# Performance work log

Measured on AMD Instinct MI355X. Metric: run time of the kernel, lower is better.

Reference implementation:

```python
import jax, jax.numpy as jnp
import numpy as np

MARGIN = 0.3

def setup_inputs() -> dict:
    key = jax.random.key(0)
    k1, k2 = jax.random.split(key)
    inputs = jax.random.normal(k1, (4096, 2048), dtype=jnp.float32)
    targets = jax.random.randint(k2, (4096,), 0, 64, dtype=jnp.int64)
    return {"inputs": inputs, "targets": targets}

def reference(inputs, targets):
    # pairwise euclidean distances: [n, n]
    sq = jnp.sum(inputs * inputs, axis=1)
    dist = sq[:, None] + sq[None, :] - 2.0 * (inputs @ inputs.T)
    dist = jnp.sqrt(jnp.clip(dist, 1e-12, None))

    mask = targets[:, None] == targets[None, :]  # same-identity mask, incl. diagonal
    neg_inf = jnp.asarray(-jnp.inf, dist.dtype)

    # soft hard-positive: softmax over positive dists, weighted sum per row
    w_ap = jax.nn.softmax(jnp.where(mask, dist, neg_inf), axis=1)
    dist_ap = jnp.sum(w_ap * dist, axis=1)  # w_ap is 0 on negatives

    # soft hard-negative: softmax over -dist restricted to negatives
    w_an = jax.nn.softmax(jnp.where(mask, neg_inf, -dist), axis=1)
    dist_an = jnp.sum(w_an * dist, axis=1)  # w_an is 0 on positives

    # MarginRankingLoss(dist_an, dist_ap, y=1): mean(max(0, dist_ap - dist_an + margin))
    return jnp.mean(jnp.maximum(dist_ap - dist_an + MARGIN, 0.0))
```

## Files before the change

### kernel.cpp

```cpp
#include <hip/hip_runtime.h>
#include <hip/hip_bf16.h>
#include <stdint.h>

#define N 4096
#define K 2048
#define BM 128
#define BN 128
#define KTB 128
#define NKT (K / KTB)
#define NCB (N / BN)
#define NRB (N / BM)
#define QS 25.4f
#define SCL2 (1.0f / (QS * QS))
#define SHIFT 64.0f

typedef int i32x4 __attribute__((ext_vector_type(4)));
typedef unsigned int u32;

__device__ __forceinline__ void gload16(const void* g, void* l) {
    __builtin_amdgcn_global_load_lds((const __attribute__((address_space(1))) u32*)g,
                                     (__attribute__((address_space(3))) u32*)l, 16, 0, 0);
}

__device__ __forceinline__ int q8(float x) {
    return __float2int_rn(fminf(fmaxf(x * QS, -127.f), 127.f));
}

__global__ __launch_bounds__(256) void k_prep(const float* __restrict__ X,
                                              char* __restrict__ Xq,
                                              float* __restrict__ sq) {
    const int row  = blockIdx.x * 4 + (threadIdx.x >> 6);
    const int lane = threadIdx.x & 63;
    const float4* xr = (const float4*)(X + (size_t)row * K);
    int* qr = (int*)(Xq + (size_t)row * K);
    float s = 0.f;
#pragma unroll
    for (int i = 0; i < 8; ++i) {
        int idx = lane + i * 64;
        float4 v = xr[idx];
        int q0 = q8(v.x), q1 = q8(v.y), q2 = q8(v.z), q3 = q8(v.w);
        s += v.x * v.x + v.y * v.y + v.z * v.z + v.w * v.w;
        qr[idx] = (q0 & 255) | ((q1 & 255) << 8) | ((q2 & 255) << 16) | ((q3 & 255) << 24);
    }
#pragma unroll
    for (int off = 32; off > 0; off >>= 1) s += __shfl_xor(s, off);
    if (lane == 0) sq[row] = s;
}

__global__ __launch_bounds__(256, 4) void k_tile(const char* __restrict__ Xq,
                                                 const int* __restrict__ tg,
                                                 const float* __restrict__ sq,
                                                 float* __restrict__ part) {
    __shared__ __align__(1024) char lds[32768];
    const int tid = threadIdx.x;
    const int cb = blockIdx.x, rb = blockIdx.y;
    const int lane = tid & 63;
    const int wid = tid >> 6;
    const int wr = wid >> 1, wc = wid & 1;
    const int l15 = lane & 15, l4 = lane >> 4;

    const int rsel = lane >> 3;
    const int csel = (lane & 7) ^ rsel;
    const char* gA = Xq + (size_t)(rb * BM + wid * 32 + rsel) * K + csel * 16;
    const char* gB = Xq + (size_t)(cb * BN + wid * 32 + rsel) * K + csel * 16;
    char* ldsA = lds + wid * 4096;
    char* ldsB = lds + 16384 + wid * 4096;

    i32x4 acc[4][4] = {};

    for (int kt = 0; kt < NKT; ++kt) {
        __syncthreads();
        const size_t ko = (size_t)kt * KTB;
#pragma unroll
        for (int j = 0; j < 4; ++j) {
            gload16(gA + ko + (size_t)j * (8 * K), ldsA + j * 1024);
            gload16(gB + ko + (size_t)j * (8 * K), ldsB + j * 1024);
        }
        __syncthreads();
#pragma unroll
        for (int ks = 0; ks < 2; ++ks) {
            i32x4 a[4], b[4];
#pragma unroll
            for (int i = 0; i < 4; ++i) {
                int ar = wr * 64 + i * 16 + l15;
                int ao = ar * 128 + ((((ks << 2) | l4) ^ (ar & 7)) << 4);
                a[i] = *(const i32x4*)(lds + ao);
                int br = wc * 64 + i * 16 + l15;
                int bo = br * 128 + ((((ks << 2) | l4) ^ (br & 7)) << 4);
                b[i] = *(const i32x4*)(lds + 16384 + bo);
            }
#pragma unroll
            for (int at = 0; at < 4; ++at)
#pragma unroll
                for (int ct = 0; ct < 4; ++ct)
                    acc[at][ct] = __builtin_amdgcn_mfma_i32_16x16x64_i8(b[ct], a[at], acc[at][ct], 0, 0, 0);
        }
    }

    float sqc[16]; int tgc[16];
#pragma unroll
    for (int ct = 0; ct < 4; ++ct)
#pragma unroll
        for (int rg = 0; rg < 4; ++rg) {
            int c = cb * BN + wc * 64 + ct * 16 + l4 * 4 + rg;
            sqc[ct * 4 + rg] = sq[c];
            tgc[ct * 4 + rg] = tg[c];
        }
#pragma unroll
    for (int at = 0; at < 4; ++at) {
        int r = rb * BM + wr * 64 + at * 16 + l15;
        float sqr = sq[r];
        int tgr = tg[r];
        float sp = 0.f, tp = 0.f, sn = 0.f, tn = 0.f;
#pragma unroll
        for (int ct = 0; ct < 4; ++ct)
#pragma unroll
            for (int rg = 0; rg < 4; ++rg) {
                float g = SCL2 * (float)acc[at][ct][rg];
                float dd = sqrtf(fmaxf(sqr + sqc[ct * 4 + rg] - 2.0f * g, 1e-12f));
                bool pos = (tgr == tgc[ct * 4 + rg]);
                float e = __expf(pos ? (dd - SHIFT) : (SHIFT - dd));
                float ed = e * dd;
                if (pos) { sp += e; tp += ed; }
                else     { sn += e; tn += ed; }
            }
#pragma unroll
        for (int off = 16; off < 64; off <<= 1) {
            sp += __shfl_xor(sp, off);
            tp += __shfl_xor(tp, off);
            sn += __shfl_xor(sn, off);
            tn += __shfl_xor(tn, off);
        }
        if (l4 == 0) {
            float4 v = {sp, tp, sn, tn};
            *(float4*)(part + (((size_t)(cb * 2 + wc) * N) + r) * 4) = v;
        }
    }
}

__global__ __launch_bounds__(256) void k_final(const float* __restrict__ part,
                                               float* __restrict__ out) {
    int r = blockIdx.x * 256 + threadIdx.x;
    float sp = 0.f, tp = 0.f, sn = 0.f, tn = 0.f;
    for (int s = 0; s < 2 * NCB; ++s) {
        float4 v = *(const float4*)(part + (((size_t)s * N) + r) * 4);
        sp += v.x; tp += v.y; sn += v.z; tn += v.w;
    }
    float h = fmaxf(tp / sp - tn / sn + 0.3f, 0.f);
    __shared__ float red[256];
    red[threadIdx.x] = h;
    __syncthreads();
    for (int k2 = 128; k2 > 0; k2 >>= 1) {
        if (threadIdx.x < k2) red[threadIdx.x] += red[threadIdx.x + k2];
        __syncthreads();
    }
    if (threadIdx.x == 0) atomicAdd(out, red[0] * (1.0f / N));
}

extern "C" void kernel_launch(void* const* d_in, const int* in_sizes, int n_in,
                              void* d_out, int out_size, void* d_ws, size_t ws_size,
                              hipStream_t stream) {
    (void)in_sizes; (void)n_in; (void)out_size; (void)ws_size;
    const float* X  = (const float*)d_in[0];
    const int*   tg = (const int*)d_in[1];

    char* ws = (char*)d_ws;
    float* sq   = (float*)ws;
    float* part = (float*)(ws + 32768);
    char*  Xq   = ws + 4227072;

    hipMemsetAsync(d_out, 0, sizeof(float), stream);
    k_prep<<<N / 4, 256, 0, stream>>>(X, Xq, sq);
    k_tile<<<dim3(NCB, NRB), 256, 0, stream>>>(Xq, tg, sq, part);
    k_final<<<N / 256, 256, 0, stream>>>(part, (float*)d_out);
}
```

Measured before the change: 64.70 us.

## Enlarge GEMM tile to 256x256 with double-buffered LDS and interleaved prefetch

The int8 Gram-matrix kernel moves from 128x128 tiles with 4 waves to 256x256 tiles with 8 waves. LDS is double-buffered at 128KB, and global-to-LDS loads for the next K tile are interleaved between MFMA phases, using explicit barriers, waitcnts and setprio. The aim is more reuse per loaded byte and overlap of memory with matrix math. The cost is a grid of only 256 blocks, higher register pressure from 32 accumulators, and lower occupancy because of the large LDS footprint.

```diff
diff --git a/kernel.cpp b/kernel.cpp
--- a/kernel.cpp
+++ b/kernel.cpp
@@ -4,12 +4,10 @@
 
 #define N 4096
 #define K 2048
-#define BM 128
-#define BN 128
+#define BT 256
 #define KTB 128
 #define NKT (K / KTB)
-#define NCB (N / BN)
-#define NRB (N / BM)
+#define NB (N / BT)
 #define QS 25.4f
 #define SCL2 (1.0f / (QS * QS))
 #define SHIFT 64.0f
@@ -47,78 +45,103 @@
     if (lane == 0) sq[row] = s;
 }
 
-__global__ __launch_bounds__(256, 4) void k_tile(const char* __restrict__ Xq,
+__global__ __launch_bounds__(512, 2) void k_tile(const char* __restrict__ Xq,
                                                  const int* __restrict__ tg,
                                                  const float* __restrict__ sq,
                                                  float* __restrict__ part) {
-    __shared__ __align__(1024) char lds[32768];
+    __shared__ __align__(1024) char lds[131072];
     const int tid = threadIdx.x;
     const int cb = blockIdx.x, rb = blockIdx.y;
     const int lane = tid & 63;
     const int wid = tid >> 6;
-    const int wr = wid >> 1, wc = wid & 1;
+    const int wm = wid >> 2, wn = wid & 3;
     const int l15 = lane & 15, l4 = lane >> 4;
 
     const int rsel = lane >> 3;
     const int csel = (lane & 7) ^ rsel;
-    const char* gA = Xq + (size_t)(rb * BM + wid * 32 + rsel) * K + csel * 16;
-    const char* gB = Xq + (size_t)(cb * BN + wid * 32 + rsel) * K + csel * 16;
-    char* ldsA = lds + wid * 4096;
-    char* ldsB = lds + 16384 + wid * 4096;
+    const char* gA0 = Xq + (size_t)(rb * BT + wid * 8 + rsel) * K + csel * 16;
+    const char* gB0 = Xq + (size_t)(cb * BT + wid * 8 + rsel) * K + csel * 16;
 
-    i32x4 acc[4][4] = {};
+#define GLOAD(j, tile, buf) \
+    gload16(((j) < 4 ? gA0 : gB0) + ((j) & 3) * (64 * K) + (size_t)(tile) * KTB, \
+            (buf) + ((j) < 4 ? 0 : 32768) + ((j) & 3) * 8192 + wid * 1024)
+
+#define RD_A(mh, ks) do { \
+    _Pragma("unroll") for (int i = 0; i < 4; ++i) { \
+        int row = wm * 128 + (mh) * 64 + i * 16 + l15; \
+        a[i] = *(const i32x4*)(bufc + row * 128 + ((((ks) * 4 + l4) ^ (row & 7)) << 4)); } \
+} while (0)
+
+#define RD_B(ks, bb) do { \
+    _Pragma("unroll") for (int i = 0; i < 4; ++i) { \
+        int row = wn * 64 + i * 16 + l15; \
+        bb[i] = *(const i32x4*)(bufc + 32768 + row * 128 + ((((ks) * 4 + l4) ^ (row & 7)) << 4)); } \
+} while (0)
+
+#define MMA(mtb, bb) do { \
+    __builtin_amdgcn_s_setprio(1); \
+    _Pragma("unroll") for (int i = 0; i < 4; ++i) \
+    _Pragma("unroll") for (int nt = 0; nt < 4; ++nt) \
+        acc[(mtb) + i][nt] = __builtin_amdgcn_mfma_i32_16x16x64_i8(bb[nt], a[i], acc[(mtb) + i][nt], 0, 0, 0); \
+    __builtin_amdgcn_s_setprio(0); \
+} while (0)
+
+#define BAR()   __builtin_amdgcn_s_barrier()
+#define LGKM0() do { asm volatile("s_waitcnt lgkmcnt(0)" ::: "memory"); \
+                     __builtin_amdgcn_sched_barrier(0); } while (0)
+#define VM0()   do { asm volatile("s_waitcnt vmcnt(0)" ::: "memory"); \
+                     __builtin_amdgcn_sched_barrier(0); } while (0)
+
+    i32x4 acc[8][4] = {};
+
+    GLOAD(0, 0, lds); GLOAD(1, 0, lds); GLOAD(2, 0, lds); GLOAD(3, 0, lds);
+    GLOAD(4, 0, lds); GLOAD(5, 0, lds); GLOAD(6, 0, lds); GLOAD(7, 0, lds);
+    VM0();
+    BAR();
 
     for (int kt = 0; kt < NKT; ++kt) {
-        __syncthreads();
-        const size_t ko = (size_t)kt * KTB;
-#pragma unroll
-        for (int j = 0; j < 4; ++j) {
-            gload16(gA + ko + (size_t)j * (8 * K), ldsA + j * 1024);
-            gload16(gB + ko + (size_t)j * (8 * K), ldsB + j * 1024);
-        }
-        __syncthreads();
-#pragma unroll
-        for (int ks = 0; ks < 2; ++ks) {
-            i32x4 a[4], b[4];
-#pragma unroll
-            for (int i = 0; i < 4; ++i) {
-                int ar = wr * 64 + i * 16 + l15;
-                int ao = ar * 128 + ((((ks << 2) | l4) ^ (ar & 7)) << 4);
-                a[i] = *(const i32x4*)(lds + ao);
-                int br = wc * 64 + i * 16 + l15;
-                int bo = br * 128 + ((((ks << 2) | l4) ^ (br & 7)) << 4);
-                b[i] = *(const i32x4*)(lds + 16384 + bo);
-            }
-#pragma unroll
-            for (int at = 0; at < 4; ++at)
-#pragma unroll
-                for (int ct = 0; ct < 4; ++ct)
-                    acc[at][ct] = __builtin_amdgcn_mfma_i32_16x16x64_i8(b[ct], a[at], acc[at][ct], 0, 0, 0);
-        }
+        const char* bufc = lds + (kt & 1) * 65536;
+        char* bufn = lds + ((kt + 1) & 1) * 65536;
+        const bool st = (kt + 1 < NKT);
+        i32x4 a[4], b0[4], b1[4];
+        RD_B(0, b0); RD_A(0, 0);
+        if (st) { GLOAD(0, kt + 1, bufn); GLOAD(1, kt + 1, bufn); }
+        BAR(); LGKM0(); MMA(0, b0); BAR();
+        RD_A(1, 0);
+        if (st) { GLOAD(2, kt + 1, bufn); GLOAD(3, kt + 1, bufn); }
+        BAR(); LGKM0(); MMA(4, b0); BAR();
+        RD_B(1, b1); RD_A(0, 1);
+        if (st) { GLOAD(4, kt + 1, bufn); GLOAD(5, kt + 1, bufn); }
+        BAR(); LGKM0(); MMA(0, b1); BAR();
+        RD_A(1, 1);
+        if (st) { GLOAD(6, kt + 1, bufn); GLOAD(7, kt + 1, bufn); }
+        BAR(); LGKM0(); MMA(4, b1);
+        VM0();
+        BAR();
     }
 
     float sqc[16]; int tgc[16];
 #pragma unroll
-    for (int ct = 0; ct < 4; ++ct)
+    for (int nt = 0; nt < 4; ++nt)
 #pragma unroll
         for (int rg = 0; rg < 4; ++rg) {
-            int c = cb * BN + wc * 64 + ct * 16 + l4 * 4 + rg;
-            sqc[ct * 4 + rg] = sq[c];
-            tgc[ct * 4 + rg] = tg[c];
+            int c = cb * BT + wn * 64 + nt * 16 + l4 * 4 + rg;
+            sqc[nt * 4 + rg] = sq[c];
+            tgc[nt * 4 + rg] = tg[c];
         }
 #pragma unroll
-    for (int at = 0; at < 4; ++at) {
-        int r = rb * BM + wr * 64 + at * 16 + l15;
+    for (int mt = 0; mt < 8; ++mt) {
+        int r = rb * BT + wm * 128 + mt * 16 + l15;
         float sqr = sq[r];
         int tgr = tg[r];
         float sp = 0.f, tp = 0.f, sn = 0.f, tn = 0.f;
 #pragma unroll
-        for (int ct = 0; ct < 4; ++ct)
+        for (int nt = 0; nt < 4; ++nt)
 #pragma unroll
             for (int rg = 0; rg < 4; ++rg) {
-                float g = SCL2 * (float)acc[at][ct][rg];
-                float dd = sqrtf(fmaxf(sqr + sqc[ct * 4 + rg] - 2.0f * g, 1e-12f));
-                bool pos = (tgr == tgc[ct * 4 + rg]);
+                float g = SCL2 * (float)acc[mt][nt][rg];
+                float dd = sqrtf(fmaxf(sqr + sqc[nt * 4 + rg] - 2.0f * g, 1e-12f));
+                bool pos = (tgr == tgc[nt * 4 + rg]);
                 float e = __expf(pos ? (dd - SHIFT) : (SHIFT - dd));
                 float ed = e * dd;
                 if (pos) { sp += e; tp += ed; }
@@ -133,7 +156,7 @@
         }
         if (l4 == 0) {
             float4 v = {sp, tp, sn, tn};
-            *(float4*)(part + (((size_t)(cb * 2 + wc) * N) + r) * 4) = v;
+            *(float4*)(part + (((size_t)(cb * 4 + wn) * N) + r) * 4) = v;
         }
     }
 }
@@ -142,7 +165,7 @@
                                                float* __restrict__ out) {
     int r = blockIdx.x * 256 + threadIdx.x;
     float sp = 0.f, tp = 0.f, sn = 0.f, tn = 0.f;
-    for (int s = 0; s < 2 * NCB; ++s) {
+    for (int s = 0; s < 64; ++s) {
         float4 v = *(const float4*)(part + (((size_t)s * N) + r) * 4);
         sp += v.x; tp += v.y; sn += v.z; tn += v.w;
     }
@@ -171,6 +194,6 @@
 
     hipMemsetAsync(d_out, 0, sizeof(float), stream);
     k_prep<<<N / 4, 256, 0, stream>>>(X, Xq, sq);
-    k_tile<<<dim3(NCB, NRB), 256, 0, stream>>>(Xq, tg, sq, part);
+    k_tile<<<dim3(NB, NB), 512, 0, stream>>>(Xq, tg, sq, part);
     k_final<<<N / 256, 256, 0, stream>>>(part, (float*)d_out);
 }
```

Measured after the change: 64.71 us. About the same (+0.0%).

## Exploit Gram matrix symmetry by computing only upper-triangular tiles

Applied to the files above, without the earlier changes.

Launches only upper-triangle tile pairs (rb<=cb) and maps the linear block index to a (rb,cb) pair with a small loop. Each off-diagonal tile computes its epilogue twice, once reduced along rows for row rb and once along columns for the transposed contribution to row cb. This roughly halves the int8 MFMA GEMM work in exchange for a heavier epilogue (double exp/sqrt) on off-diagonal tiles and a serial index-decode loop. Partial slots are laid out so each row still receives exactly 2*NRB contributions.

```diff
diff --git a/kernel.cpp b/kernel.cpp
--- a/kernel.cpp
+++ b/kernel.cpp
@@ -5,11 +5,11 @@
 #define N 4096
 #define K 2048
 #define BM 128
-#define BN 128
 #define KTB 128
 #define NKT (K / KTB)
-#define NCB (N / BN)
 #define NRB (N / BM)
+#define NTILES (NRB * (NRB + 1) / 2)
+#define SLOTS (2 * NRB)
 #define QS 25.4f
 #define SCL2 (1.0f / (QS * QS))
 #define SHIFT 64.0f
@@ -53,7 +53,10 @@
                                                  float* __restrict__ part) {
     __shared__ __align__(1024) char lds[32768];
     const int tid = threadIdx.x;
-    const int cb = blockIdx.x, rb = blockIdx.y;
+    int tt = blockIdx.x, rb = 0;
+    while (tt >= NRB - rb) { tt -= NRB - rb; ++rb; }
+    const int cb = rb + tt;
+
     const int lane = tid & 63;
     const int wid = tid >> 6;
     const int wr = wid >> 1, wc = wid & 1;
@@ -62,7 +65,7 @@
     const int rsel = lane >> 3;
     const int csel = (lane & 7) ^ rsel;
     const char* gA = Xq + (size_t)(rb * BM + wid * 32 + rsel) * K + csel * 16;
-    const char* gB = Xq + (size_t)(cb * BN + wid * 32 + rsel) * K + csel * 16;
+    const char* gB = Xq + (size_t)(cb * BM + wid * 32 + rsel) * K + csel * 16;
     char* ldsA = lds + wid * 4096;
     char* ldsB = lds + 16384 + wid * 4096;
 
@@ -102,23 +105,28 @@
     for (int ct = 0; ct < 4; ++ct)
 #pragma unroll
         for (int rg = 0; rg < 4; ++rg) {
-            int c = cb * BN + wc * 64 + ct * 16 + l4 * 4 + rg;
+            int c = cb * BM + wc * 64 + ct * 16 + l4 * 4 + rg;
             sqc[ct * 4 + rg] = sq[c];
             tgc[ct * 4 + rg] = tg[c];
         }
+    float sqr[4]; int tgr[4];
 #pragma unroll
     for (int at = 0; at < 4; ++at) {
         int r = rb * BM + wr * 64 + at * 16 + l15;
-        float sqr = sq[r];
-        int tgr = tg[r];
+        sqr[at] = sq[r];
+        tgr[at] = tg[r];
+    }
+
+#pragma unroll
+    for (int at = 0; at < 4; ++at) {
         float sp = 0.f, tp = 0.f, sn = 0.f, tn = 0.f;
 #pragma unroll
         for (int ct = 0; ct < 4; ++ct)
 #pragma unroll
             for (int rg = 0; rg < 4; ++rg) {
                 float g = SCL2 * (float)acc[at][ct][rg];
-                float dd = sqrtf(fmaxf(sqr + sqc[ct * 4 + rg] - 2.0f * g, 1e-12f));
-                bool pos = (tgr == tgc[ct * 4 + rg]);
+                float dd = sqrtf(fmaxf(sqr[at] + sqc[ct * 4 + rg] - 2.0f * g, 1e-12f));
+                bool pos = (tgr[at] == tgc[ct * 4 + rg]);
                 float e = __expf(pos ? (dd - SHIFT) : (SHIFT - dd));
                 float ed = e * dd;
                 if (pos) { sp += e; tp += ed; }
@@ -132,9 +140,43 @@
             tn += __shfl_xor(tn, off);
         }
         if (l4 == 0) {
+            int r = rb * BM + wr * 64 + at * 16 + l15;
             float4 v = {sp, tp, sn, tn};
             *(float4*)(part + (((size_t)(cb * 2 + wc) * N) + r) * 4) = v;
         }
+    }
+
+    if (cb != rb) {
+#pragma unroll
+        for (int ct = 0; ct < 4; ++ct)
+#pragma unroll
+            for (int rg = 0; rg < 4; ++rg) {
+                float cS = sqc[ct * 4 + rg];
+                int   cT = tgc[ct * 4 + rg];
+                float sp = 0.f, tp = 0.f, sn = 0.f, tn = 0.f;
+#pragma unroll
+                for (int at = 0; at < 4; ++at) {
+                    float g = SCL2 * (float)acc[at][ct][rg];
+                    float dd = sqrtf(fmaxf(sqr[at] + cS - 2.0f * g, 1e-12f));
+                    bool pos = (tgr[at] == cT);
+                    float e = __expf(pos ? (dd - SHIFT) : (SHIFT - dd));
+                    float ed = e * dd;
+                    if (pos) { sp += e; tp += ed; }
+                    else     { sn += e; tn += ed; }
+                }
+#pragma unroll
+                for (int off = 1; off < 16; off <<= 1) {
+                    sp += __shfl_xor(sp, off);
+                    tp += __shfl_xor(tp, off);
+                    sn += __shfl_xor(sn, off);
+                    tn += __shfl_xor(tn, off);
+                }
+                if (l15 == 0) {
+                    int c = cb * BM + wc * 64 + ct * 16 + l4 * 4 + rg;
+                    float4 v = {sp, tp, sn, tn};
+                    *(float4*)(part + (((size_t)(rb * 2 + wr) * N) + c) * 4) = v;
+                }
+            }
     }
 }
 
@@ -142,7 +184,7 @@
                                                float* __restrict__ out) {
     int r = blockIdx.x * 256 + threadIdx.x;
     float sp = 0.f, tp = 0.f, sn = 0.f, tn = 0.f;
-    for (int s = 0; s < 2 * NCB; ++s) {
+    for (int s = 0; s < SLOTS; ++s) {
         float4 v = *(const float4*)(part + (((size_t)s * N) + r) * 4);
         sp += v.x; tp += v.y; sn += v.z; tn += v.w;
     }
@@ -171,6 +213,6 @@
 
     hipMemsetAsync(d_out, 0, sizeof(float), stream);
     k_prep<<<N / 4, 256, 0, stream>>>(X, Xq, sq);
-    k_tile<<<dim3(NCB, NRB), 256, 0, stream>>>(Xq, tg, sq, part);
+    k_tile<<<NTILES, 256, 0, stream>>>(Xq, tg, sq, part);
     k_final<<<N / 256, 256, 0, stream>>>(part, (float*)d_out);
 }
```

Result: slower. 66.30 us (+2.5%).

## Switch to 32x32x32 int8 MFMA and remap blocks for XCD-aware L2 locality

Applied to the files above, without the earlier changes.

Replaces the 16x16x64 int8 MFMA tiling with 32x32x32 int8 MFMA (2x2 accumulators of 16 ints per wave) and rewrites LDS fragment loads and the epilogue to match the new output layout. It also flattens the grid and maps block IDs so that each of the 8 XCDs works on a contiguous patch of row and column tiles, aiming for better L2 reuse of the quantized operands. The epilogue now needs only one cross-lane shuffle step per row instead of two. The larger MFMA may lower issue overhead but changes register pressure and the LDS read pattern.

```diff
diff --git a/kernel.cpp b/kernel.cpp
--- a/kernel.cpp
+++ b/kernel.cpp
@@ -5,16 +5,15 @@
 #define N 4096
 #define K 2048
 #define BM 128
-#define BN 128
 #define KTB 128
 #define NKT (K / KTB)
-#define NCB (N / BN)
 #define NRB (N / BM)
 #define QS 25.4f
 #define SCL2 (1.0f / (QS * QS))
 #define SHIFT 64.0f
 
 typedef int i32x4 __attribute__((ext_vector_type(4)));
+typedef int i32x16 __attribute__((ext_vector_type(16)));
 typedef unsigned int u32;
 
 __device__ __forceinline__ void gload16(const void* g, void* l) {
@@ -53,20 +52,24 @@
                                                  float* __restrict__ part) {
     __shared__ __align__(1024) char lds[32768];
     const int tid = threadIdx.x;
-    const int cb = blockIdx.x, rb = blockIdx.y;
+    const int L = blockIdx.x;
+    const int xcd = L & 7, w = L >> 3;
+    const int rb = (xcd & 3) * 8 + (w & 7);
+    const int cb = (xcd >> 2) * 16 + (w >> 3);
+
     const int lane = tid & 63;
     const int wid = tid >> 6;
     const int wr = wid >> 1, wc = wid & 1;
-    const int l15 = lane & 15, l4 = lane >> 4;
+    const int l31 = lane & 31, lh = lane >> 5;
 
     const int rsel = lane >> 3;
     const int csel = (lane & 7) ^ rsel;
     const char* gA = Xq + (size_t)(rb * BM + wid * 32 + rsel) * K + csel * 16;
-    const char* gB = Xq + (size_t)(cb * BN + wid * 32 + rsel) * K + csel * 16;
+    const char* gB = Xq + (size_t)(cb * BM + wid * 32 + rsel) * K + csel * 16;
     char* ldsA = lds + wid * 4096;
     char* ldsB = lds + 16384 + wid * 4096;
 
-    i32x4 acc[4][4] = {};
+    i32x16 acc[2][2] = {};
 
     for (int kt = 0; kt < NKT; ++kt) {
         __syncthreads();
@@ -78,61 +81,61 @@
         }
         __syncthreads();
 #pragma unroll
-        for (int ks = 0; ks < 2; ++ks) {
-            i32x4 a[4], b[4];
+        for (int ks = 0; ks < 4; ++ks) {
+            i32x4 a[2], b[2];
 #pragma unroll
-            for (int i = 0; i < 4; ++i) {
-                int ar = wr * 64 + i * 16 + l15;
-                int ao = ar * 128 + ((((ks << 2) | l4) ^ (ar & 7)) << 4);
-                a[i] = *(const i32x4*)(lds + ao);
-                int br = wc * 64 + i * 16 + l15;
-                int bo = br * 128 + ((((ks << 2) | l4) ^ (br & 7)) << 4);
-                b[i] = *(const i32x4*)(lds + 16384 + bo);
+            for (int i = 0; i < 2; ++i) {
+                int ar = wr * 64 + i * 32 + l31;
+                a[i] = *(const i32x4*)(lds + ar * 128 + (((ks * 2 + lh) ^ (ar & 7)) << 4));
+                int br = wc * 64 + i * 32 + l31;
+                b[i] = *(const i32x4*)(lds + 16384 + br * 128 + (((ks * 2 + lh) ^ (br & 7)) << 4));
             }
 #pragma unroll
-            for (int at = 0; at < 4; ++at)
+            for (int at = 0; at < 2; ++at)
 #pragma unroll
-                for (int ct = 0; ct < 4; ++ct)
-                    acc[at][ct] = __builtin_amdgcn_mfma_i32_16x16x64_i8(b[ct], a[at], acc[at][ct], 0, 0, 0);
+                for (int ct = 0; ct < 2; ++ct)
+                    acc[at][ct] = __builtin_amdgcn_mfma_i32_32x32x32_i8(b[ct], a[at], acc[at][ct], 0, 0, 0);
         }
     }
 
-    float sqc[16]; int tgc[16];
+    float sqr[2]; int tgr[2];
 #pragma unroll
-    for (int ct = 0; ct < 4; ++ct)
+    for (int at = 0; at < 2; ++at) {
+        int r = rb * BM + wr * 64 + at * 32 + l31;
+        sqr[at] = sq[r];
+        tgr[at] = tg[r];
+    }
+    float sp[2] = {0.f, 0.f}, tp[2] = {0.f, 0.f};
+    float sn[2] = {0.f, 0.f}, tn[2] = {0.f, 0.f};
 #pragma unroll
-        for (int rg = 0; rg < 4; ++rg) {
-            int c = cb * BN + wc * 64 + ct * 16 + l4 * 4 + rg;
-            sqc[ct * 4 + rg] = sq[c];
-            tgc[ct * 4 + rg] = tg[c];
-        }
+    for (int reg = 0; reg < 16; ++reg) {
+        const int cidx = (reg & 3) + 8 * (reg >> 2) + 4 * lh;
 #pragma unroll
-    for (int at = 0; at < 4; ++at) {
-        int r = rb * BM + wr * 64 + at * 16 + l15;
-        float sqr = sq[r];
-        int tgr = tg[r];
-        float sp = 0.f, tp = 0.f, sn = 0.f, tn = 0.f;
+        for (int ct = 0; ct < 2; ++ct) {
+            int c = cb * BM + wc * 64 + ct * 32 + cidx;
+            float sc = sq[c];
+            int   tc = tg[c];
 #pragma unroll
-        for (int ct = 0; ct < 4; ++ct)
-#pragma unroll
-            for (int rg = 0; rg < 4; ++rg) {
-                float g = SCL2 * (float)acc[at][ct][rg];
-                float dd = sqrtf(fmaxf(sqr + sqc[ct * 4 + rg] - 2.0f * g, 1e-12f));
-                bool pos = (tgr == tgc[ct * 4 + rg]);
+            for (int at = 0; at < 2; ++at) {
+                float g = SCL2 * (float)acc[at][ct][reg];
+                float dd = sqrtf(fmaxf(sqr[at] + sc - 2.0f * g, 1e-12f));
+                bool pos = (tgr[at] == tc);
                 float e = __expf(pos ? (dd - SHIFT) : (SHIFT - dd));
                 float ed = e * dd;
-                if (pos) { sp += e; tp += ed; }
-                else     { sn += e; tn += ed; }
+                if (pos) { sp[at] += e; tp[at] += ed; }
+                else     { sn[at] += e; tn[at] += ed; }
             }
+        }
+    }
 #pragma unroll
-        for (int off = 16; off < 64; off <<= 1) {
-            sp += __shfl_xor(sp, off);
-            tp += __shfl_xor(tp, off);
-            sn += __shfl_xor(sn, off);
-            tn += __shfl_xor(tn, off);
-        }
-        if (l4 == 0) {
-            float4 v = {sp, tp, sn, tn};
+    for (int at = 0; at < 2; ++at) {
+        sp[at] += __shfl_xor(sp[at], 32);
+        tp[at] += __shfl_xor(tp[at], 32);
+        sn[at] += __shfl_xor(sn[at], 32);
+        tn[at] += __shfl_xor(tn[at], 32);
+        if (lh == 0) {
+            int r = rb * BM + wr * 64 + at * 32 + l31;
+            float4 v = {sp[at], tp[at], sn[at], tn[at]};
             *(float4*)(part + (((size_t)(cb * 2 + wc) * N) + r) * 4) = v;
         }
     }
@@ -142,7 +145,7 @@
                                                float* __restrict__ out) {
     int r = blockIdx.x * 256 + threadIdx.x;
     float sp = 0.f, tp = 0.f, sn = 0.f, tn = 0.f;
-    for (int s = 0; s < 2 * NCB; ++s) {
+    for (int s = 0; s < 2 * NRB; ++s) {
         float4 v = *(const float4*)(part + (((size_t)s * N) + r) * 4);
         sp += v.x; tp += v.y; sn += v.z; tn += v.w;
     }
@@ -171,6 +174,6 @@
 
     hipMemsetAsync(d_out, 0, sizeof(float), stream);
     k_prep<<<N / 4, 256, 0, stream>>>(X, Xq, sq);
-    k_tile<<<dim3(NCB, NRB), 256, 0, stream>>>(Xq, tg, sq, part);
+    k_tile<<<NRB * NRB, 256, 0, stream>>>(Xq, tg, sq, part);
     k_final<<<N / 256, 256, 0, stream>>>(part, (float*)d_out);
 }
```

After: 69.04 us. 1.07x slower.
